# Optimization experiments

Hardware: AMD Instinct MI355X
Metric: run time of the kernel (lower is better)

Reference implementation:

```python
import jax, jax.numpy as jnp
import numpy as np

B, T, S, D, H, HD, DFF, NB = 2, 2048, 2048, 768, 12, 64, 3072, 32
HID = H * HD
EPS = 1e-6
NEG = -1e9


def rmsnorm(x, w):
    # T5 RMSNorm: no mean subtraction, no bias
    var = jnp.mean(jnp.square(x), axis=-1, keepdims=True)
    return x * jax.lax.rsqrt(var + EPS) * w


def sdpa(h, kv, m, wq, wk, wv, wo):
    # h: [B,Tq,D], kv: [B,Tk,D], m: additive mask broadcastable to [B,H,Tq,Tk]
    b, tq, _ = h.shape
    tk = kv.shape[1]
    q = (h @ wq).reshape(b, tq, H, HD)
    k = (kv @ wk).reshape(b, tk, H, HD)
    v = (kv @ wv).reshape(b, tk, H, HD)
    scores = jnp.einsum('bthd,bshd->bhts', q, k) + m  # scale=1.0 (T5)
    p = jax.nn.softmax(scores, axis=-1)
    y = jnp.einsum('bhts,bshd->bthd', p, v).reshape(b, tq, HID)
    return y @ wo


def setup_inputs() -> dict:
    key = jax.random.key(0)
    ks = jax.random.split(key, 16)
    x = jax.random.normal(ks[0], (B, T, D), dtype=jnp.float32)
    # causal additive mask for decoder self-attention
    causal = jnp.tril(jnp.ones((T, T), dtype=bool))
    mask = jnp.broadcast_to(jnp.where(causal, 0.0, NEG)[None, None], (B, 1, T, T)).astype(jnp.float32)
    relative_position = jax.random.randint(ks[1], (1, 1, T, T), 0, NB)
    encoder_hidden_states = jax.random.normal(ks[2], (B, S, D), dtype=jnp.float32)
    encoder_attention_mask = jnp.zeros((B, 1, T, S), dtype=jnp.float32)
    sc = 0.02
    p = {
        'sn_w': jnp.ones((D,), jnp.float32),
        'wq': sc * jax.random.normal(ks[3], (D, HID)),
        'wk': sc * jax.random.normal(ks[4], (D, HID)),
        'wv': sc * jax.random.normal(ks[5], (D, HID)),
        'wo': sc * jax.random.normal(ks[6], (HID, D)),
        'rel_emb': sc * jax.random.normal(ks[7], (NB, H)),
        'cn_w': jnp.ones((D,), jnp.float32),
        'cwq': sc * jax.random.normal(ks[8], (D, HID)),
        'cwk': sc * jax.random.normal(ks[9], (D, HID)),
        'cwv': sc * jax.random.normal(ks[10], (D, HID)),
        'cwo': sc * jax.random.normal(ks[11], (HID, D)),
        'pn_w': jnp.ones((D,), jnp.float32),
        'ffn_wi': sc * jax.random.normal(ks[12], (D, DFF)),
        'ffn_wo': sc * jax.random.normal(ks[13], (DFF, D)),
    }
    return dict(x=x, mask=mask, relative_position=relative_position,
                encoder_hidden_states=encoder_hidden_states,
                encoder_attention_mask=encoder_attention_mask, **p)


def reference(x, mask, relative_position, encoder_hidden_states, encoder_attention_mask,
              sn_w, wq, wk, wv, wo, rel_emb, cn_w, cwq, cwk, cwv, cwo, pn_w, ffn_wi, ffn_wo):
    # self-attention with relative-position bias added into additive mask
    h = rmsnorm(x, sn_w)
    # rel_emb[relative_position]: [1,1,T,T,H] -> permute(0,1,4,2,3) -> squeeze(0) -> [1,H,T,T]
    position_bias = jnp.transpose(rel_emb[relative_position], (0, 1, 4, 2, 3))[0]
    self_mask = mask + position_bias
    y = sdpa(h, h, self_mask, wq, wk, wv, wo)
    attn_out = y + x
    # cross-attention (no relative bias -> zeros position bias)
    enc_dec_position_bias = jnp.zeros_like(encoder_attention_mask)
    h2 = rmsnorm(attn_out, cn_w)
    y2 = sdpa(h2, encoder_hidden_states, encoder_attention_mask + enc_dec_position_bias,
              cwq, cwk, cwv, cwo)
    attn_out = y2 + attn_out
    # T5 FFN: relu(x @ wi) @ wo, pre-norm, residual
    hn = rmsnorm(attn_out, pn_w)
    ff = jax.nn.relu(hn @ ffn_wi) @ ffn_wo
    return (attn_out + ff, position_bias, enc_dec_position_bias)
```

## Files before the change

kernel.cpp:

```cpp
#include <hip/hip_runtime.h>
#include <hip/hip_bf16.h>
#include <stdint.h>

#define T5_B   2
#define T5_T   2048
#define T5_S   2048
#define T5_D   768
#define T5_H   12
#define T5_HD  64
#define T5_DFF 3072
#define T5_NB  32
#define NROW   4096

#define LOG2E 1.4426950408889634f

typedef __attribute__((ext_vector_type(8))) short bf16x8;
typedef __attribute__((ext_vector_type(4))) short short4v;
typedef __attribute__((ext_vector_type(4))) float f32x4;
typedef __attribute__((ext_vector_type(16))) float f32x16;

__device__ __forceinline__ unsigned short f2bf(float x) {
  unsigned int u = __float_as_uint(x);
  unsigned int r = (u + 0x7FFFu + ((u >> 16) & 1u)) >> 16;
  return (unsigned short)r;
}

__device__ __forceinline__ float fexp2(float x) {
  float d;
  asm("v_exp_f32 %0, %1" : "=v"(d) : "v"(x));
  return d;
}

__device__ __forceinline__ void load_lds16(const void* g, void* l) {
  __builtin_amdgcn_global_load_lds(
      (__attribute__((address_space(1))) void*)(const_cast<void*>(g)),
      (__attribute__((address_space(3))) void*)(l), 16, 0, 0);
}

__device__ __forceinline__ unsigned cvt_pk_bf16(float lo_, float hi_) {
  unsigned d;
  asm("v_cvt_pk_bf16_f32 %0, %1, %2" : "=v"(d) : "v"(lo_), "v"(hi_));
  return d;
}

__device__ __forceinline__ f32x4 mfma16(short4v a, short4v b, f32x4 c) {
#if __has_builtin(__builtin_amdgcn_mfma_f32_16x16x16bf16_1k)
  return __builtin_amdgcn_mfma_f32_16x16x16bf16_1k(a, b, c, 0, 0, 0);
#else
  asm volatile("v_mfma_f32_16x16x16_bf16 %0, %1, %2, %0" : "+v"(c) : "v"(a), "v"(b));
  return c;
#endif
}

__device__ __forceinline__ int xcd_swz(int f, int nwg) {
  int q8 = nwg >> 3, r8 = nwg & 7, xcd = f & 7, base = f >> 3;
  return (xcd < r8 ? xcd * (q8 + 1) : r8 * (q8 + 1) + (xcd - r8) * q8) + base;
}

template <int TM, int TN, int EPI, int NBUF>
__device__ __forceinline__ void gemm_body(
    int f, int gx, int nwg,
    const unsigned short* __restrict__ A, const unsigned short* __restrict__ Bt,
    void* __restrict__ C, const float* __restrict__ res, int N, int K,
    unsigned short* LDS, unsigned short* vtp = nullptr, int vcol0 = 0, int qe = 0) {
  constexpr bool USE32 = (TM >= 128 && TN >= 128);
  constexpr int WR = (TM >= 128) ? 2 : 1;
  constexpr int WC = 4 / WR;
  constexpr int AM = TM / WR / 16;
  constexpr int AN = TN / WC / 16;
  constexpr int CHA = TM / 8, CHB = TN / 8, CPW = (CHA + CHB) / 4;
  constexpr int BUFSH = (TM + TN) * 64;
  constexpr int DEPTH = NBUF - 1;
  const int tid = threadIdx.x, lane = tid & 63, wv = tid >> 6;
  const int lo = lane & 15, hi = lane >> 4;
  const int l5 = lane >> 5, l31 = lane & 31;
  const int wr = wv / WC, wc = wv % WC;
  const int wg = xcd_swz(f, nwg);
  const int m0 = (wg / gx) * TM, n0 = (wg % gx) * TN;

  f32x4 acc[USE32 ? 1 : AM][USE32 ? 1 : AN];
  f32x16 acc32[USE32 ? 2 : 1][USE32 ? 2 : 1];
  if (USE32) {
#pragma unroll
    for (int i = 0; i < (USE32 ? 2 : 1); ++i)
#pragma unroll
      for (int j = 0; j < (USE32 ? 2 : 1); ++j)
#pragma unroll
        for (int r = 0; r < 16; ++r) acc32[i][j][r] = 0.f;
  } else {
#pragma unroll
    for (int i = 0; i < (USE32 ? 1 : AM); ++i)
#pragma unroll
      for (int j = 0; j < (USE32 ? 1 : AN); ++j) acc[i][j] = f32x4{0.f, 0.f, 0.f, 0.f};
  }

  const int srr  = lane >> 3;
  const int scol = ((lane & 7) ^ srr) * 8;

  auto stage = [&](int k0, int bsel) {
    unsigned short* Ab = LDS + bsel * BUFSH;
    unsigned short* Bb = Ab + TM * 64;
#pragma unroll
    for (int j = 0; j < CPW; ++j) {
      int c = wv * CPW + j;
      if (c < CHA)
        load_lds16(A + (size_t)(m0 + c * 8 + srr) * K + k0 + scol, Ab + c * 512);
      else {
        int c2 = c - CHA;
        load_lds16(Bt + (size_t)(n0 + c2 * 8 + srr) * K + k0 + scol, Bb + c2 * 512);
      }
    }
  };

  const int nIt = K >> 6;
#pragma unroll
  for (int p = 0; p < DEPTH; ++p)
    if (p < nIt) stage(p << 6, p % NBUF);

  for (int it = 0; it < nIt; ++it) {
    const int bsel = it % NBUF;
    if (NBUF == 1) {
      stage(it << 6, 0);
      asm volatile("s_waitcnt vmcnt(0)" ::: "memory");
    } else if (it + DEPTH < nIt) {
      stage((it + DEPTH) << 6, (it + DEPTH) % NBUF);
      asm volatile("s_waitcnt vmcnt(%0)" :: "n"(DEPTH * CPW) : "memory");
    } else if (it + 1 < nIt) {
      asm volatile("s_waitcnt vmcnt(%0)" :: "n"(CPW) : "memory");
    } else {
      asm volatile("s_waitcnt vmcnt(0)" ::: "memory");
    }
    __builtin_amdgcn_s_barrier();
    __builtin_amdgcn_sched_barrier(0);
    const unsigned short* Ab = LDS + bsel * BUFSH;
    const unsigned short* Bb = Ab + TM * 64;
    if (USE32) {
#pragma unroll
      for (int kk = 0; kk < 4; ++kk) {
        bf16x8 af[2], bfr[2];
#pragma unroll
        for (int i = 0; i < 2; ++i) {
          int row = wr * 64 + i * 32 + l31;
          unsigned by = (unsigned)(row * 128) + ((unsigned)(((kk * 2 + l5) ^ (row & 7))) << 4);
          af[i] = *(const bf16x8*)((const char*)Ab + by);
        }
#pragma unroll
        for (int j = 0; j < 2; ++j) {
          int row = wc * 64 + j * 32 + l31;
          unsigned by = (unsigned)(row * 128) + ((unsigned)(((kk * 2 + l5) ^ (row & 7))) << 4);
          bfr[j] = *(const bf16x8*)((const char*)Bb + by);
        }
        __builtin_amdgcn_s_setprio(1);
#pragma unroll
        for (int i = 0; i < 2; ++i)
#pragma unroll
          for (int j = 0; j < 2; ++j)
            acc32[i][j] = __builtin_amdgcn_mfma_f32_32x32x16_bf16(af[i], bfr[j], acc32[i][j], 0, 0, 0);
        __builtin_amdgcn_s_setprio(0);
      }
    } else {
#pragma unroll
      for (int kk = 0; kk < 2; ++kk) {
        bf16x8 af[AM], bfr[AN];
#pragma unroll
        for (int i = 0; i < AM; ++i) {
          int row = wr * (AM * 16) + i * 16 + lo;
          unsigned by = (unsigned)(row * 128) + ((unsigned)(((kk * 4 + hi) ^ (row & 7))) << 4);
          af[i] = *(const bf16x8*)((const char*)Ab + by);
        }
#pragma unroll
        for (int j = 0; j < AN; ++j) {
          int row = wc * (AN * 16) + j * 16 + lo;
          unsigned by = (unsigned)(row * 128) + ((unsigned)(((kk * 4 + hi) ^ (row & 7))) << 4);
          bfr[j] = *(const bf16x8*)((const char*)Bb + by);
        }
        __builtin_amdgcn_s_setprio(1);
#pragma unroll
        for (int i = 0; i < AM; ++i)
#pragma unroll
          for (int j = 0; j < AN; ++j)
            acc[i][j] = __builtin_amdgcn_mfma_f32_16x16x32_bf16(af[i], bfr[j], acc[i][j], 0, 0, 0);
        __builtin_amdgcn_s_setprio(0);
      }
    }
    __builtin_amdgcn_sched_barrier(0);
    __builtin_amdgcn_s_barrier();
  }

  if (USE32) {
#pragma unroll
    for (int i = 0; i < 2; ++i)
#pragma unroll
      for (int j = 0; j < 2; ++j) {
        int colb = n0 + wc * 64 + j * 32 + l31;
#pragma unroll
        for (int g = 0; g < 4; ++g) {
          int rowb = m0 + wr * 64 + i * 32 + g * 8 + 4 * l5;
          if (EPI == 3 && colb >= vcol0) {
            int cc = colb - vcol0, hh = cc >> 6, dd = cc & 63;
            int bb = rowb >> 11, tt = rowb & 2047;
            unsigned long long pk = (unsigned long long)f2bf(acc32[i][j][g * 4 + 0])
                                  | ((unsigned long long)f2bf(acc32[i][j][g * 4 + 1]) << 16)
                                  | ((unsigned long long)f2bf(acc32[i][j][g * 4 + 2]) << 32)
                                  | ((unsigned long long)f2bf(acc32[i][j][g * 4 + 3]) << 48);
            *(unsigned long long*)(vtp + ((size_t)((bb * 12 + hh) * 64 + dd)) * 2048 + tt) = pk;
          } else {
#pragma unroll
            for (int rr = 0; rr < 4; ++rr) {
              float v = acc32[i][j][g * 4 + rr];
              size_t idx = (size_t)(rowb + rr) * N + colb;
              if (EPI == 3) {
                if (colb < qe) v *= LOG2E;
                ((unsigned short*)C)[idx] = f2bf(v);
              } else if (EPI == 0) {
                ((unsigned short*)C)[idx] = f2bf(v);
              } else if (EPI == 1) {
                ((float*)C)[idx] = v + res[idx];
              } else if (EPI == 2) {
                ((unsigned short*)C)[idx] = f2bf(fmaxf(v, 0.0f));
              } else {
                ((unsigned short*)C)[idx] = f2bf(v * LOG2E);
              }
            }
          }
        }
      }
  } else {
#pragma unroll
    for (int mi = 0; mi < (USE32 ? 1 : AM); ++mi)
#pragma unroll
      for (int ni = 0; ni < (USE32 ? 1 : AN); ++ni) {
        int row = m0 + wr * (AM * 16) + mi * 16 + hi * 4;
        int col = n0 + wc * (AN * 16) + ni * 16 + lo;
#pragma unroll
        for (int r = 0; r < 4; ++r) {
          float v = acc[mi][ni][r];
          size_t idx = (size_t)(row + r) * N + col;
          if (EPI == 0 || EPI == 3) {
            ((unsigned short*)C)[idx] = f2bf(v);
          } else if (EPI == 1) {
            ((float*)C)[idx] = v + res[idx];
          } else if (EPI == 2) {
            ((unsigned short*)C)[idx] = f2bf(fmaxf(v, 0.0f));
          } else {
            ((unsigned short*)C)[idx] = f2bf(v * LOG2E);
          }
        }
      }
  }
}

template <int TM, int TN, int EPI, int NBUF>
__global__ __launch_bounds__(256)
void gemm_bt(const unsigned short* __restrict__ A, const unsigned short* __restrict__ Bt,
             void* __restrict__ C, const float* __restrict__ res, int N, int K) {
  __shared__ __align__(16) unsigned short LDS[NBUF * (TM + TN) * 64];
  int f = blockIdx.y * gridDim.x + blockIdx.x;
  gemm_body<TM, TN, EPI, NBUF>(f, gridDim.x, gridDim.x * gridDim.y, A, Bt, C, res, N, K, LDS);
}

struct PrepArgs {
  const float* wsrc[10];
  unsigned short* wdst[10];
  const float* enc; unsigned short* encb;
  const int* rp; unsigned char* rp8;
  const float* x; const float* snw; unsigned short* normb;
};

__global__ __launch_bounds__(256)
void prep_kernel(PrepArgs a) {
  __shared__ __align__(16) float tile[32][33];
  const int bid = blockIdx.x, tid = threadIdx.x;
  if (bid < 9216) {
    int widx, rem, Kd, Nd;
    if (bid < 4608)      { widx = bid / 576; rem = bid % 576;  Kd = 768;  Nd = 768;  }
    else if (bid < 6912) { widx = 8;         rem = bid - 4608; Kd = 768;  Nd = 3072; }
    else                 { widx = 9;         rem = bid - 6912; Kd = 3072; Nd = 768;  }
    const float* W = a.wsrc[widx];
    unsigned short* Wt = a.wdst[widx];
    int nb = Nd / 32;
    int n0 = (rem % nb) * 32, k0 = (rem / nb) * 32;
    int tx = tid & 31, ty = tid >> 5;
#pragma unroll
    for (int i = 0; i < 32; i += 8)
      tile[ty + i][tx] = W[(size_t)(k0 + ty + i) * Nd + n0 + tx];
    __syncthreads();
#pragma unroll
    for (int i = 0; i < 32; i += 8)
      Wt[(size_t)(n0 + ty + i) * Kd + k0 + tx] = f2bf(tile[tx][ty + i]);
  } else if (bid < 12288) {
    int i = (bid - 9216) * 256 + tid;
    float4 v = ((const float4*)a.enc)[i];
    unsigned long long pk = (unsigned long long)f2bf(v.x)
                          | ((unsigned long long)f2bf(v.y) << 16)
                          | ((unsigned long long)f2bf(v.z) << 32)
                          | ((unsigned long long)f2bf(v.w) << 48);
    *(unsigned long long*)(a.encb + (size_t)i * 4) = pk;
  } else if (bid < 13312) {
    int idx = (bid - 12288) * 256 + tid;
    const int4* src = (const int4*)(a.rp + (size_t)idx * 16);
    int4 v0 = src[0], v1 = src[1], v2 = src[2], v3 = src[3];
    uint4 o;
    o.x = (v0.x & 31) | ((v0.y & 31) << 8) | ((v0.z & 31) << 16) | ((v0.w & 31) << 24);
    o.y = (v1.x & 31) | ((v1.y & 31) << 8) | ((v1.z & 31) << 16) | ((v1.w & 31) << 24);
    o.z = (v2.x & 31) | ((v2.y & 31) << 8) | ((v2.z & 31) << 16) | ((v2.w & 31) << 24);
    o.w = (v3.x & 31) | ((v3.y & 31) << 8) | ((v3.z & 31) << 16) | ((v3.w & 31) << 24);
    ((uint4*)a.rp8)[idx] = o;
  } else {
    int row = bid - 13312;
    const float* r = a.x + (size_t)row * 768;
    float x0 = r[tid], x1 = r[tid + 256], x2 = r[tid + 512];
    float s = x0 * x0 + x1 * x1 + x2 * x2;
#pragma unroll
    for (int off = 32; off > 0; off >>= 1) s += __shfl_xor(s, off);
    float* wsm = &tile[0][0];
    int lane = tid & 63, wvv = tid >> 6;
    if (lane == 0) wsm[wvv] = s;
    __syncthreads();
    float tot = wsm[0] + wsm[1] + wsm[2] + wsm[3];
    float rinv = rsqrtf(tot * (1.0f / 768.0f) + 1e-6f);
    unsigned short* o = a.normb + (size_t)row * 768;
    o[tid]       = f2bf(x0 * rinv * a.snw[tid]);
    o[tid + 256] = f2bf(x1 * rinv * a.snw[tid + 256]);
    o[tid + 512] = f2bf(x2 * rinv * a.snw[tid + 512]);
  }
}

__global__ __launch_bounds__(256)
void rmsnorm_kernel(const float* __restrict__ in, const float* __restrict__ w,
                    unsigned short* __restrict__ out) {
  int row = blockIdx.x, tid = threadIdx.x;
  const float* r = in + (size_t)row * 768;
  float x0 = r[tid], x1 = r[tid + 256], x2 = r[tid + 512];
  float s = x0 * x0 + x1 * x1 + x2 * x2;
#pragma unroll
  for (int off = 32; off > 0; off >>= 1) s += __shfl_xor(s, off);
  __shared__ float ws_[4];
  int lane = tid & 63, wv = tid >> 6;
  if (lane == 0) ws_[wv] = s;
  __syncthreads();
  float tot = ws_[0] + ws_[1] + ws_[2] + ws_[3];
  float rinv = rsqrtf(tot * (1.0f / 768.0f) + 1e-6f);
  unsigned short* o = out + (size_t)row * 768;
  o[tid]       = f2bf(x0 * rinv * w[tid]);
  o[tid + 256] = f2bf(x1 * rinv * w[tid + 256]);
  o[tid + 512] = f2bf(x2 * rinv * w[tid + 512]);
}

struct Stage1Args {
  const unsigned short *normb, *wqkvT, *encb, *wckvT;
  unsigned short *qkv, *ckv, *vT1, *vT2;
  const int* rp; const float* rel;
  float *out1, *out2;
};

__global__ __launch_bounds__(256)
void stage1_kernel(Stage1Args a) {
  __shared__ __align__(16) unsigned short LDS[16384];
  const int bid = blockIdx.x, tid = threadIdx.x;
  if (bid < 576) {
    gemm_body<128, 128, 3, 1>(bid, 18, 576, a.normb, a.wqkvT, a.qkv, nullptr, 2304, 768,
                              LDS, a.vT1, 1536, 768);
  } else if (bid < 960) {
    gemm_body<128, 128, 3, 1>(bid - 576, 12, 384, a.encb, a.wckvT, a.ckv, nullptr, 1536, 768,
                              LDS, a.vT2, 768, 0);
  } else {
    const int p = bid - 960;
    float* rl = (float*)LDS;
    for (int i = tid; i < 384; i += 256) rl[i] = a.rel[i];
    __syncthreads();
    int t = p >> 1;
    int s = (p & 1) * 1024 + tid * 4;
    int4 nb = *(const int4*)(a.rp + (size_t)t * 2048 + s);
#pragma unroll
    for (int h = 0; h < 12; ++h) {
      float4 v = make_float4(rl[nb.x * 12 + h], rl[nb.y * 12 + h],
                             rl[nb.z * 12 + h], rl[nb.w * 12 + h]);
      *(float4*)(a.out1 + ((size_t)h * 2048 + t) * 2048 + s) = v;
    }
    size_t zbase = ((size_t)p * 256 + tid) * 8;
    float4 z = make_float4(0.f, 0.f, 0.f, 0.f);
    *(float4*)(a.out2 + zbase)     = z;
    *(float4*)(a.out2 + zbase + 4) = z;
  }
}

template <bool SELF>
__device__ __forceinline__ void attn_qcomp(
    const bf16x8& qf0, const bf16x8& qf1, f32x4* Oc, float& l_,
    const unsigned* nb4, const float* rel_l, int qrow, bool edge, int s0,
    const unsigned short* Kb, const unsigned short* Vb, int lo, int hi) {
  f32x4 S[4];
  __builtin_amdgcn_s_setprio(1);
#pragma unroll
  for (int ct = 0; ct < 4; ++ct) {
    int krow = ct * 16 + lo;
    unsigned by0 = ((unsigned)(krow * 128 + hi * 16))      ^ ((unsigned)(krow & 7) << 4);
    unsigned by1 = ((unsigned)(krow * 128 + 64 + hi * 16)) ^ ((unsigned)(krow & 7) << 4);
    bf16x8 kf0 = *(const bf16x8*)((const char*)Kb + by0);
    bf16x8 kf1 = *(const bf16x8*)((const char*)Kb + by1);
    f32x4 sa = f32x4{0.f, 0.f, 0.f, 0.f};
    sa = __builtin_amdgcn_mfma_f32_16x16x32_bf16(kf0, qf0, sa, 0, 0, 0);
    sa = __builtin_amdgcn_mfma_f32_16x16x32_bf16(kf1, qf1, sa, 0, 0, 0);
    S[ct] = sa;
  }
  __builtin_amdgcn_s_setprio(0);

  if constexpr (SELF) {
#pragma unroll
    for (int ct = 0; ct < 4; ++ct) {
#pragma unroll
      for (int r = 0; r < 4; ++r) {
        int s = s0 + ct * 16 + hi * 4 + r;
        float sc = S[ct][r] + rel_l[(nb4[ct] >> (8 * r)) & 31u];
        if (edge && s > qrow) sc = -1e30f;
        S[ct][r] = sc;
      }
    }
  }

  float rs = 0.f;
#pragma unroll
  for (int ct = 0; ct < 4; ++ct)
#pragma unroll
    for (int r = 0; r < 4; ++r) { float e = fexp2(S[ct][r]); S[ct][r] = e; rs += e; }
  l_ += rs;

  short4v pf[4];
#pragma unroll
  for (int ct = 0; ct < 4; ++ct) {
    union { unsigned u[2]; short4v s; } cv;
    cv.u[0] = cvt_pk_bf16(S[ct][0], S[ct][1]);
    cv.u[1] = cvt_pk_bf16(S[ct][2], S[ct][3]);
    pf[ct] = cv.s;
  }

  __builtin_amdgcn_s_setprio(1);
#pragma unroll
  for (int dt = 0; dt < 4; ++dt) {
    int vrow = dt * 16 + lo;
#pragma unroll
    for (int ct = 0; ct < 4; ++ct) {
      unsigned vb = ((unsigned)(vrow * 128 + ct * 32 + hi * 8)) ^ ((unsigned)(vrow & 7) << 4);
      short4v vf = *(const short4v*)((const char*)Vb + vb);
      Oc[dt] = mfma16(vf, pf[ct], Oc[dt]);
    }
  }
  __builtin_amdgcn_s_setprio(0);
}

__device__ __forceinline__ void attn_store(f32x4* Oc, float l_, unsigned short* yr) {
  l_ += __shfl_xor(l_, 16);
  l_ += __shfl_xor(l_, 32);
  float inv = 1.0f / l_;
#pragma unroll
  for (int dt = 0; dt < 4; ++dt) {
    unsigned long long pk = (unsigned long long)f2bf(Oc[dt][0] * inv)
                          | ((unsigned long long)f2bf(Oc[dt][1] * inv) << 16)
                          | ((unsigned long long)f2bf(Oc[dt][2] * inv) << 32)
                          | ((unsigned long long)f2bf(Oc[dt][3] * inv) << 48);
    *(unsigned long long*)(yr + dt * 16) = pk;
  }
}

__global__ __launch_bounds__(256)
void attn_self_kernel(const unsigned short* __restrict__ qp,
                      const unsigned short* __restrict__ kp,
                      const unsigned short* __restrict__ vT,
                      const unsigned char* __restrict__ rp8,
                      const float* __restrict__ rel_emb,
                      unsigned short* __restrict__ yp) {
  __shared__ __align__(16) unsigned short Kls[2][4096];
  __shared__ __align__(16) unsigned short Vls[2][4096];
  __shared__ float rel_l[32];

  const int tid = threadIdx.x, lane = tid & 63, wv = tid >> 6;
  const int lo = lane & 15, hi = lane >> 4;
  const int wg = xcd_swz(blockIdx.x + 16 * (blockIdx.y + 12 * blockIdx.z), 384);
  const int xq = wg & 15, h = (wg >> 4) % 12, b = (wg >> 4) / 12;
  const int qta = xq, qtb = 31 - xq;
  const int ntiles = qtb + 1;

  if (tid < 32) rel_l[tid] = rel_emb[tid * 12 + h] * LOG2E;

  const int qA = qta * 64 + wv * 16 + lo;
  const int qB = qtb * 64 + wv * 16 + lo;
  const unsigned short* qrA = qp + (size_t)(b * T5_T + qA) * 2304 + h * 64 + hi * 8;
  const unsigned short* qrB = qp + (size_t)(b * T5_T + qB) * 2304 + h * 64 + hi * 8;
  const bf16x8 qa0 = *(const bf16x8*)qrA;
  const bf16x8 qa1 = *(const bf16x8*)(qrA + 32);
  const bf16x8 qb0 = *(const bf16x8*)qrB;
  const bf16x8 qb1 = *(const bf16x8*)(qrB + 32);
  const unsigned char* rpqA = rp8 + (size_t)qA * 2048 + hi * 4;
  const unsigned char* rpqB = rp8 + (size_t)qB * 2048 + hi * 4;

  f32x4 OA[4], OB[4];
  float lA = 0.f, lB = 0.f;
#pragma unroll
  for (int i = 0; i < 4; ++i) { OA[i] = f32x4{0.f, 0.f, 0.f, 0.f}; OB[i] = f32x4{0.f, 0.f, 0.f, 0.f}; }

  const int krr = lane >> 3;
  const int kd0 = ((lane & 7) ^ krr) * 8;

  auto stage = [&](int kt, int bsel) {
    const int s0 = kt * 64;
#pragma unroll
    for (int j = 0; j < 2; ++j) {
      int c = wv * 2 + j;
      int rr = c * 8 + krr;
      load_lds16(kp + (size_t)(b * 2048 + s0 + rr) * 2304 + h * 64 + kd0, &Kls[bsel][c * 512]);
      load_lds16(vT + (size_t)((b * 12 + h) * 64 + rr) * 2048 + s0 + kd0,  &Vls[bsel][c * 512]);
    }
  };

  stage(0, 0);

  for (int kt = 0; kt < ntiles; ++kt) {
    const int bsel = kt & 1;
    const int s0 = kt * 64;
    asm volatile("s_waitcnt vmcnt(0)" ::: "memory");
    __syncthreads();
    unsigned nbA[4], nbB[4];
    if (kt <= qta) {
#pragma unroll
      for (int ct = 0; ct < 4; ++ct) nbA[ct] = *(const unsigned*)(rpqA + s0 + ct * 16);
    }
#pragma unroll
    for (int ct = 0; ct < 4; ++ct) nbB[ct] = *(const unsigned*)(rpqB + s0 + ct * 16);
    if (kt + 1 < ntiles) stage(kt + 1, bsel ^ 1);

    const unsigned short* Kb = &Kls[bsel][0];
    const unsigned short* Vb = &Vls[bsel][0];

    if (kt <= qta)
      attn_qcomp<true>(qa0, qa1, OA, lA, nbA, rel_l, qA, kt == qta, s0, Kb, Vb, lo, hi);
    attn_qcomp<true>(qb0, qb1, OB, lB, nbB, rel_l, qB, kt == qtb, s0, Kb, Vb, lo, hi);
  }

#if !__has_builtin(__builtin_amdgcn_mfma_f32_16x16x16bf16_1k)
  asm volatile("s_nop 7\n\ts_nop 7" ::: );
#endif

  attn_store(OA, lA, yp + (size_t)(b * T5_T + qA) * 768 + h * 64 + hi * 4);
  attn_store(OB, lB, yp + (size_t)(b * T5_T + qB) * 768 + h * 64 + hi * 4);
}

__global__ __launch_bounds__(256)
void attn_cross_kernel(const unsigned short* __restrict__ qp,
                       const unsigned short* __restrict__ kp,
                       const unsigned short* __restrict__ vT,
                       unsigned short* __restrict__ yp) {
  __shared__ __align__(16) unsigned short Kls[2][4096];
  __shared__ __align__(16) unsigned short Vls[2][4096];

  const int tid = threadIdx.x, lane = tid & 63, wv = tid >> 6;
  const int lo = lane & 15, hi = lane >> 4;
  const int wg = xcd_swz(blockIdx.x + 16 * (blockIdx.y + 12 * blockIdx.z), 384);
  const int xq = wg & 15, h = (wg >> 4) % 12, b = (wg >> 4) / 12;

  const int qA = (xq * 2) * 64 + wv * 16 + lo;
  const int qB = (xq * 2 + 1) * 64 + wv * 16 + lo;
  const unsigned short* qrA = qp + (size_t)(b * T5_T + qA) * 768 + h * 64 + hi * 8;
  const unsigned short* qrB = qp + (size_t)(b * T5_T + qB) * 768 + h * 64 + hi * 8;
  const bf16x8 qa0 = *(const bf16x8*)qrA;
  const bf16x8 qa1 = *(const bf16x8*)(qrA + 32);
  const bf16x8 qb0 = *(const bf16x8*)qrB;
  const bf16x8 qb1 = *(const bf16x8*)(qrB + 32);

  f32x4 OA[4], OB[4];
  float lA = 0.f, lB = 0.f;
#pragma unroll
  for (int i = 0; i < 4; ++i) { OA[i] = f32x4{0.f, 0.f, 0.f, 0.f}; OB[i] = f32x4{0.f, 0.f, 0.f, 0.f}; }

  const int krr = lane >> 3;
  const int kd0 = ((lane & 7) ^ krr) * 8;

  auto stage = [&](int kt, int bsel) {
    const int s0 = kt * 64;
#pragma unroll
    for (int j = 0; j < 2; ++j) {
      int c = wv * 2 + j;
      int rr = c * 8 + krr;
      load_lds16(kp + (size_t)(b * 2048 + s0 + rr) * 1536 + h * 64 + kd0, &Kls[bsel][c * 512]);
      load_lds16(vT + (size_t)((b * 12 + h) * 64 + rr) * 2048 + s0 + kd0, &Vls[bsel][c * 512]);
    }
  };

  stage(0, 0);

  for (int kt = 0; kt < 32; ++kt) {
    const int bsel = kt & 1;
    asm volatile("s_waitcnt vmcnt(0)" ::: "memory");
    __syncthreads();
    if (kt + 1 < 32) stage(kt + 1, bsel ^ 1);
    const unsigned short* Kb = &Kls[bsel][0];
    const unsigned short* Vb = &Vls[bsel][0];
    attn_qcomp<false>(qa0, qa1, OA, lA, nullptr, nullptr, 0, false, kt * 64, Kb, Vb, lo, hi);
    attn_qcomp<false>(qb0, qb1, OB, lB, nullptr, nullptr, 0, false, kt * 64, Kb, Vb, lo, hi);
  }

#if !__has_builtin(__builtin_amdgcn_mfma_f32_16x16x16bf16_1k)
  asm volatile("s_nop 7\n\ts_nop 7" ::: );
#endif

  attn_store(OA, lA, yp + (size_t)(b * T5_T + qA) * 768 + h * 64 + hi * 4);
  attn_store(OB, lB, yp + (size_t)(b * T5_T + qB) * 768 + h * 64 + hi * 4);
}

extern "C" void kernel_launch(void* const* d_in, const int* in_sizes, int n_in,
                              void* d_out, int out_size, void* d_ws, size_t ws_size,
                              hipStream_t stream) {
  (void)in_sizes; (void)n_in; (void)out_size; (void)ws_size;
  const float* x    = (const float*)d_in[0];
  const int*   rp   = (const int*)d_in[2];
  const float* enc  = (const float*)d_in[3];
  const float* sn_w = (const float*)d_in[5];
  const float* wq   = (const float*)d_in[6];
  const float* wk   = (const float*)d_in[7];
  const float* wvw  = (const float*)d_in[8];
  const float* wo   = (const float*)d_in[9];
  const float* rel  = (const float*)d_in[10];
  const float* cn_w = (const float*)d_in[11];
  const float* cwq  = (const float*)d_in[12];
  const float* cwk  = (const float*)d_in[13];
  const float* cwv  = (const float*)d_in[14];
  const float* cwo  = (const float*)d_in[15];
  const float* pn_w = (const float*)d_in[16];
  const float* wi   = (const float*)d_in[17];
  const float* wo2  = (const float*)d_in[18];

  float* out0 = (float*)d_out;
  float* out1 = out0 + (size_t)NROW * T5_D;
  float* out2 = out1 + (size_t)T5_H * T5_T * T5_T;

  char* ws = (char*)d_ws;
  size_t off = 0;
  auto alloc = [&](size_t bytes) { char* p = ws + off; off += (bytes + 255) & ~(size_t)255; return p; };
  unsigned short* wqkvT = (unsigned short*)alloc((size_t)2304 * 768 * 2);
  unsigned short* woT   = (unsigned short*)alloc((size_t)768 * 768 * 2);
  unsigned short* wckvT = (unsigned short*)alloc((size_t)1536 * 768 * 2);
  unsigned short* wcqT  = (unsigned short*)alloc((size_t)768 * 768 * 2);
  unsigned short* wcoT  = (unsigned short*)alloc((size_t)768 * 768 * 2);
  unsigned short* wiT   = (unsigned short*)alloc((size_t)3072 * 768 * 2);
  unsigned short* woT2  = (unsigned short*)alloc((size_t)768 * 3072 * 2);
  unsigned short* normb = (unsigned short*)alloc((size_t)NROW * 768 * 2);
  unsigned short* encb  = (unsigned short*)alloc((size_t)NROW * 768 * 2);
  unsigned short* ybuf  = (unsigned short*)alloc((size_t)NROW * 768 * 2);
  unsigned short* cq    = (unsigned short*)alloc((size_t)NROW * 768 * 2);
  float*          attn  = (float*)alloc((size_t)NROW * 768 * 4);
  unsigned char*  rp8p  = (unsigned char*)alloc((size_t)2048 * 2048);
  unsigned short* qkv   = (unsigned short*)alloc((size_t)NROW * 2304 * 2);
  unsigned short* ckv   = (unsigned short*)alloc((size_t)NROW * 1536 * 2);
  unsigned short* vT1   = (unsigned short*)alloc((size_t)24 * 64 * 2048 * 2);
  unsigned short* vT2   = (unsigned short*)alloc((size_t)24 * 64 * 2048 * 2);
  unsigned short* ffh   = (unsigned short*)alloc((size_t)NROW * 3072 * 2);

  dim3 blk(256);

  {
    PrepArgs pa;
    pa.wsrc[0] = wq;  pa.wdst[0] = wqkvT;
    pa.wsrc[1] = wk;  pa.wdst[1] = wqkvT + 768 * 768;
    pa.wsrc[2] = wvw; pa.wdst[2] = wqkvT + 2 * 768 * 768;
    pa.wsrc[3] = wo;  pa.wdst[3] = woT;
    pa.wsrc[4] = cwk; pa.wdst[4] = wckvT;
    pa.wsrc[5] = cwv; pa.wdst[5] = wckvT + 768 * 768;
    pa.wsrc[6] = cwq; pa.wdst[6] = wcqT;
    pa.wsrc[7] = cwo; pa.wdst[7] = wcoT;
    pa.wsrc[8] = wi;  pa.wdst[8] = wiT;
    pa.wsrc[9] = wo2; pa.wdst[9] = woT2;
    pa.enc = enc; pa.encb = encb; pa.rp = rp; pa.rp8 = rp8p;
    pa.x = x; pa.snw = sn_w; pa.normb = normb;
    prep_kernel<<<17408, blk, 0, stream>>>(pa);
  }

  {
    Stage1Args sa;
    sa.normb = normb; sa.wqkvT = wqkvT; sa.encb = encb; sa.wckvT = wckvT;
    sa.qkv = qkv; sa.ckv = ckv; sa.vT1 = vT1; sa.vT2 = vT2;
    sa.rp = rp; sa.rel = rel; sa.out1 = out1; sa.out2 = out2;
    stage1_kernel<<<5056, blk, 0, stream>>>(sa);
  }

  attn_self_kernel<<<dim3(16, 12, 2), blk, 0, stream>>>(qkv, qkv + 768, vT1, rp8p, rel, ybuf);
  gemm_bt<64, 64, 1, 3><<<dim3(12, 64), blk, 0, stream>>>(ybuf, woT, attn, x, 768, 768);

  rmsnorm_kernel<<<NROW, blk, 0, stream>>>(attn, cn_w, normb);
  gemm_bt<64, 64, 4, 3><<<dim3(12, 64), blk, 0, stream>>>(normb, wcqT, cq, nullptr, 768, 768);
  attn_cross_kernel<<<dim3(16, 12, 2), blk, 0, stream>>>(cq, ckv, vT2, ybuf);
  gemm_bt<64, 64, 1, 3><<<dim3(12, 64), blk, 0, stream>>>(ybuf, wcoT, attn, attn, 768, 768);

  rmsnorm_kernel<<<NROW, blk, 0, stream>>>(attn, pn_w, normb);
  gemm_bt<128, 128, 2, 1><<<dim3(24, 32), blk, 0, stream>>>(normb, wiT, ffh, nullptr, 3072, 768);
  gemm_bt<64, 64, 1, 3><<<dim3(12, 64), blk, 0, stream>>>(ffh, woT2, out0, attn, 768, 3072);
}
```

Before: 340.9 us.

## Split attention query tiles across 512-thread blocks and defer weight prep to stage1

The self- and cross-attention kernels move from 256-thread blocks, where each wave handled two query tiles in sequence, to 512-thread blocks, where each group of four waves owns one query tile. This gives more waves per block to hide latency and halves the per-wave serial work and register footprint, while each K/V tile staged in LDS is still shared by both query tiles. Transposing the weights that are not needed for the first GEMMs (wo, cwq, cwo, ffn) and packing the relative positions are moved out of the prep kernel into the stage1 kernel, so they overlap with the QKV GEMMs instead of delaying them. In the causal kernel the waves on the short query tile sit idle for the later key tiles, and the larger blocks may reduce occupancy.

```diff
diff --git a/kernel.cpp b/kernel.cpp
--- a/kernel.cpp
+++ b/kernel.cpp
@@ -55,6 +55,22 @@
 __device__ __forceinline__ int xcd_swz(int f, int nwg) {
   int q8 = nwg >> 3, r8 = nwg & 7, xcd = f & 7, base = f >> 3;
   return (xcd < r8 ? xcd * (q8 + 1) : r8 * (q8 + 1) + (xcd - r8) * q8) + base;
+}
+
+__device__ __forceinline__ void wtrans_tile(const float* __restrict__ W,
+                                            unsigned short* __restrict__ Wt,
+                                            int rem, int Kd, int Nd,
+                                            float (*tile)[33], int tid) {
+  int nb = Nd / 32;
+  int n0 = (rem % nb) * 32, k0 = (rem / nb) * 32;
+  int tx = tid & 31, ty = tid >> 5;
+#pragma unroll
+  for (int i = 0; i < 32; i += 8)
+    tile[ty + i][tx] = W[(size_t)(k0 + ty + i) * Nd + n0 + tx];
+  __syncthreads();
+#pragma unroll
+  for (int i = 0; i < 32; i += 8)
+    Wt[(size_t)(n0 + ty + i) * Kd + k0 + tx] = f2bf(tile[tx][ty + i]);
 }
 
 template <int TM, int TN, int EPI, int NBUF>
@@ -260,10 +276,9 @@
 }
 
 struct PrepArgs {
-  const float* wsrc[10];
-  unsigned short* wdst[10];
+  const float* wsrc[5];
+  unsigned short* wdst[5];
   const float* enc; unsigned short* encb;
-  const int* rp; unsigned char* rp8;
   const float* x; const float* snw; unsigned short* normb;
 };
 
@@ -271,43 +286,19 @@
 void prep_kernel(PrepArgs a) {
   __shared__ __align__(16) float tile[32][33];
   const int bid = blockIdx.x, tid = threadIdx.x;
-  if (bid < 9216) {
-    int widx, rem, Kd, Nd;
-    if (bid < 4608)      { widx = bid / 576; rem = bid % 576;  Kd = 768;  Nd = 768;  }
-    else if (bid < 6912) { widx = 8;         rem = bid - 4608; Kd = 768;  Nd = 3072; }
-    else                 { widx = 9;         rem = bid - 6912; Kd = 3072; Nd = 768;  }
-    const float* W = a.wsrc[widx];
-    unsigned short* Wt = a.wdst[widx];
-    int nb = Nd / 32;
-    int n0 = (rem % nb) * 32, k0 = (rem / nb) * 32;
-    int tx = tid & 31, ty = tid >> 5;
-#pragma unroll
-    for (int i = 0; i < 32; i += 8)
-      tile[ty + i][tx] = W[(size_t)(k0 + ty + i) * Nd + n0 + tx];
-    __syncthreads();
-#pragma unroll
-    for (int i = 0; i < 32; i += 8)
-      Wt[(size_t)(n0 + ty + i) * Kd + k0 + tx] = f2bf(tile[tx][ty + i]);
-  } else if (bid < 12288) {
-    int i = (bid - 9216) * 256 + tid;
+  if (bid < 2880) {
+    int widx = bid / 576, rem = bid % 576;
+    wtrans_tile(a.wsrc[widx], a.wdst[widx], rem, 768, 768, tile, tid);
+  } else if (bid < 5952) {
+    int i = (bid - 2880) * 256 + tid;
     float4 v = ((const float4*)a.enc)[i];
     unsigned long long pk = (unsigned long long)f2bf(v.x)
                           | ((unsigned long long)f2bf(v.y) << 16)
                           | ((unsigned long long)f2bf(v.z) << 32)
                           | ((unsigned long long)f2bf(v.w) << 48);
     *(unsigned long long*)(a.encb + (size_t)i * 4) = pk;
-  } else if (bid < 13312) {
-    int idx = (bid - 12288) * 256 + tid;
-    const int4* src = (const int4*)(a.rp + (size_t)idx * 16);
-    int4 v0 = src[0], v1 = src[1], v2 = src[2], v3 = src[3];
-    uint4 o;
-    o.x = (v0.x & 31) | ((v0.y & 31) << 8) | ((v0.z & 31) << 16) | ((v0.w & 31) << 24);
-    o.y = (v1.x & 31) | ((v1.y & 31) << 8) | ((v1.z & 31) << 16) | ((v1.w & 31) << 24);
-    o.z = (v2.x & 31) | ((v2.y & 31) << 8) | ((v2.z & 31) << 16) | ((v2.w & 31) << 24);
-    o.w = (v3.x & 31) | ((v3.y & 31) << 8) | ((v3.z & 31) << 16) | ((v3.w & 31) << 24);
-    ((uint4*)a.rp8)[idx] = o;
   } else {
-    int row = bid - 13312;
+    int row = bid - 5952;
     const float* r = a.x + (size_t)row * 768;
     float x0 = r[tid], x1 = r[tid + 256], x2 = r[tid + 512];
     float s = x0 * x0 + x1 * x1 + x2 * x2;
@@ -352,6 +343,9 @@
   unsigned short *qkv, *ckv, *vT1, *vT2;
   const int* rp; const float* rel;
   float *out1, *out2;
+  const float *wo, *cwq, *cwo, *wi, *wo2;
+  unsigned short *woT, *wcqT, *wcoT, *wiT, *woT2;
+  unsigned char* rp8;
 };
 
 __global__ __launch_bounds__(256)
@@ -364,7 +358,7 @@
   } else if (bid < 960) {
     gemm_body<128, 128, 3, 1>(bid - 576, 12, 384, a.encb, a.wckvT, a.ckv, nullptr, 1536, 768,
                               LDS, a.vT2, 768, 0);
-  } else {
+  } else if (bid < 5056) {
     const int p = bid - 960;
     float* rl = (float*)LDS;
     for (int i = tid; i < 384; i += 256) rl[i] = a.rel[i];
@@ -382,6 +376,26 @@
     float4 z = make_float4(0.f, 0.f, 0.f, 0.f);
     *(float4*)(a.out2 + zbase)     = z;
     *(float4*)(a.out2 + zbase + 4) = z;
+  } else if (bid < 5632) {
+    wtrans_tile(a.wo,  a.woT,  bid - 5056, 768, 768, (float(*)[33])LDS, tid);
+  } else if (bid < 6208) {
+    wtrans_tile(a.cwq, a.wcqT, bid - 5632, 768, 768, (float(*)[33])LDS, tid);
+  } else if (bid < 6784) {
+    wtrans_tile(a.cwo, a.wcoT, bid - 6208, 768, 768, (float(*)[33])LDS, tid);
+  } else if (bid < 9088) {
+    wtrans_tile(a.wi,  a.wiT,  bid - 6784, 768, 3072, (float(*)[33])LDS, tid);
+  } else if (bid < 11392) {
+    wtrans_tile(a.wo2, a.woT2, bid - 9088, 3072, 768, (float(*)[33])LDS, tid);
+  } else {
+    int idx = (bid - 11392) * 256 + tid;
+    const int4* src = (const int4*)(a.rp + (size_t)idx * 16);
+    int4 v0 = src[0], v1 = src[1], v2 = src[2], v3 = src[3];
+    uint4 o;
+    o.x = (v0.x & 31) | ((v0.y & 31) << 8) | ((v0.z & 31) << 16) | ((v0.w & 31) << 24);
+    o.y = (v1.x & 31) | ((v1.y & 31) << 8) | ((v1.z & 31) << 16) | ((v1.w & 31) << 24);
+    o.z = (v2.x & 31) | ((v2.y & 31) << 8) | ((v2.z & 31) << 16) | ((v2.w & 31) << 24);
+    o.w = (v3.x & 31) | ((v3.y & 31) << 8) | ((v3.z & 31) << 16) | ((v3.w & 31) << 24);
+    ((uint4*)a.rp8)[idx] = o;
   }
 }
 
@@ -463,7 +477,7 @@
   }
 }
 
-__global__ __launch_bounds__(256)
+__global__ __launch_bounds__(512)
 void attn_self_kernel(const unsigned short* __restrict__ qp,
                       const unsigned short* __restrict__ kp,
                       const unsigned short* __restrict__ vT,
@@ -476,41 +490,34 @@
 
   const int tid = threadIdx.x, lane = tid & 63, wv = tid >> 6;
   const int lo = lane & 15, hi = lane >> 4;
+  const int qset = wv >> 2, wq = wv & 3;
   const int wg = xcd_swz(blockIdx.x + 16 * (blockIdx.y + 12 * blockIdx.z), 384);
   const int xq = wg & 15, h = (wg >> 4) % 12, b = (wg >> 4) / 12;
   const int qta = xq, qtb = 31 - xq;
   const int ntiles = qtb + 1;
+  const int qt = qset ? qtb : qta;
 
   if (tid < 32) rel_l[tid] = rel_emb[tid * 12 + h] * LOG2E;
 
-  const int qA = qta * 64 + wv * 16 + lo;
-  const int qB = qtb * 64 + wv * 16 + lo;
-  const unsigned short* qrA = qp + (size_t)(b * T5_T + qA) * 2304 + h * 64 + hi * 8;
-  const unsigned short* qrB = qp + (size_t)(b * T5_T + qB) * 2304 + h * 64 + hi * 8;
-  const bf16x8 qa0 = *(const bf16x8*)qrA;
-  const bf16x8 qa1 = *(const bf16x8*)(qrA + 32);
-  const bf16x8 qb0 = *(const bf16x8*)qrB;
-  const bf16x8 qb1 = *(const bf16x8*)(qrB + 32);
-  const unsigned char* rpqA = rp8 + (size_t)qA * 2048 + hi * 4;
-  const unsigned char* rpqB = rp8 + (size_t)qB * 2048 + hi * 4;
-
-  f32x4 OA[4], OB[4];
-  float lA = 0.f, lB = 0.f;
-#pragma unroll
-  for (int i = 0; i < 4; ++i) { OA[i] = f32x4{0.f, 0.f, 0.f, 0.f}; OB[i] = f32x4{0.f, 0.f, 0.f, 0.f}; }
+  const int q = qt * 64 + wq * 16 + lo;
+  const unsigned short* qr = qp + (size_t)(b * T5_T + q) * 2304 + h * 64 + hi * 8;
+  const bf16x8 qf0 = *(const bf16x8*)qr;
+  const bf16x8 qf1 = *(const bf16x8*)(qr + 32);
+  const unsigned char* rpq = rp8 + (size_t)q * 2048 + hi * 4;
+
+  f32x4 Oc[4];
+  float l_ = 0.f;
+#pragma unroll
+  for (int i = 0; i < 4; ++i) Oc[i] = f32x4{0.f, 0.f, 0.f, 0.f};
 
   const int krr = lane >> 3;
   const int kd0 = ((lane & 7) ^ krr) * 8;
 
   auto stage = [&](int kt, int bsel) {
     const int s0 = kt * 64;
-#pragma unroll
-    for (int j = 0; j < 2; ++j) {
-      int c = wv * 2 + j;
-      int rr = c * 8 + krr;
-      load_lds16(kp + (size_t)(b * 2048 + s0 + rr) * 2304 + h * 64 + kd0, &Kls[bsel][c * 512]);
-      load_lds16(vT + (size_t)((b * 12 + h) * 64 + rr) * 2048 + s0 + kd0,  &Vls[bsel][c * 512]);
-    }
+    int rr = wv * 8 + krr;
+    load_lds16(kp + (size_t)(b * 2048 + s0 + rr) * 2304 + h * 64 + kd0, &Kls[bsel][wv * 512]);
+    load_lds16(vT + (size_t)((b * 12 + h) * 64 + rr) * 2048 + s0 + kd0,  &Vls[bsel][wv * 512]);
   };
 
   stage(0, 0);
@@ -520,32 +527,27 @@
     const int s0 = kt * 64;
     asm volatile("s_waitcnt vmcnt(0)" ::: "memory");
     __syncthreads();
-    unsigned nbA[4], nbB[4];
-    if (kt <= qta) {
-#pragma unroll
-      for (int ct = 0; ct < 4; ++ct) nbA[ct] = *(const unsigned*)(rpqA + s0 + ct * 16);
+    const bool active = qset || (kt <= qta);
+    unsigned nb4[4];
+    if (active) {
+#pragma unroll
+      for (int ct = 0; ct < 4; ++ct) nb4[ct] = *(const unsigned*)(rpq + s0 + ct * 16);
     }
-#pragma unroll
-    for (int ct = 0; ct < 4; ++ct) nbB[ct] = *(const unsigned*)(rpqB + s0 + ct * 16);
     if (kt + 1 < ntiles) stage(kt + 1, bsel ^ 1);
 
-    const unsigned short* Kb = &Kls[bsel][0];
-    const unsigned short* Vb = &Vls[bsel][0];
-
-    if (kt <= qta)
-      attn_qcomp<true>(qa0, qa1, OA, lA, nbA, rel_l, qA, kt == qta, s0, Kb, Vb, lo, hi);
-    attn_qcomp<true>(qb0, qb1, OB, lB, nbB, rel_l, qB, kt == qtb, s0, Kb, Vb, lo, hi);
+    if (active)
+      attn_qcomp<true>(qf0, qf1, Oc, l_, nb4, rel_l, q, kt == qt, s0,
+                       &Kls[bsel][0], &Vls[bsel][0], lo, hi);
   }
 
 #if !__has_builtin(__builtin_amdgcn_mfma_f32_16x16x16bf16_1k)
   asm volatile("s_nop 7\n\ts_nop 7" ::: );
 #endif
 
-  attn_store(OA, lA, yp + (size_t)(b * T5_T + qA) * 768 + h * 64 + hi * 4);
-  attn_store(OB, lB, yp + (size_t)(b * T5_T + qB) * 768 + h * 64 + hi * 4);
-}
-
-__global__ __launch_bounds__(256)
+  attn_store(Oc, l_, yp + (size_t)(b * T5_T + q) * 768 + h * 64 + hi * 4);
+}
+
+__global__ __launch_bounds__(512)
 void attn_cross_kernel(const unsigned short* __restrict__ qp,
                        const unsigned short* __restrict__ kp,
                        const unsigned short* __restrict__ vT,
@@ -555,35 +557,28 @@
 
   const int tid = threadIdx.x, lane = tid & 63, wv = tid >> 6;
   const int lo = lane & 15, hi = lane >> 4;
+  const int qset = wv >> 2, wq = wv & 3;
   const int wg = xcd_swz(blockIdx.x + 16 * (blockIdx.y + 12 * blockIdx.z), 384);
   const int xq = wg & 15, h = (wg >> 4) % 12, b = (wg >> 4) / 12;
 
-  const int qA = (xq * 2) * 64 + wv * 16 + lo;
-  const int qB = (xq * 2 + 1) * 64 + wv * 16 + lo;
-  const unsigned short* qrA = qp + (size_t)(b * T5_T + qA) * 768 + h * 64 + hi * 8;
-  const unsigned short* qrB = qp + (size_t)(b * T5_T + qB) * 768 + h * 64 + hi * 8;
-  const bf16x8 qa0 = *(const bf16x8*)qrA;
-  const bf16x8 qa1 = *(const bf16x8*)(qrA + 32);
-  const bf16x8 qb0 = *(const bf16x8*)qrB;
-  const bf16x8 qb1 = *(const bf16x8*)(qrB + 32);
-
-  f32x4 OA[4], OB[4];
-  float lA = 0.f, lB = 0.f;
-#pragma unroll
-  for (int i = 0; i < 4; ++i) { OA[i] = f32x4{0.f, 0.f, 0.f, 0.f}; OB[i] = f32x4{0.f, 0.f, 0.f, 0.f}; }
+  const int q = (xq * 2 + qset) * 64 + wq * 16 + lo;
+  const unsigned short* qr = qp + (size_t)(b * T5_T + q) * 768 + h * 64 + hi * 8;
+  const bf16x8 qf0 = *(const bf16x8*)qr;
+  const bf16x8 qf1 = *(const bf16x8*)(qr + 32);
+
+  f32x4 Oc[4];
+  float l_ = 0.f;
+#pragma unroll
+  for (int i = 0; i < 4; ++i) Oc[i] = f32x4{0.f, 0.f, 0.f, 0.f};
 
   const int krr = lane >> 3;
   const int kd0 = ((lane & 7) ^ krr) * 8;
 
   auto stage = [&](int kt, int bsel) {
     const int s0 = kt * 64;
-#pragma unroll
-    for (int j = 0; j < 2; ++j) {
-      int c = wv * 2 + j;
-      int rr = c * 8 + krr;
-      load_lds16(kp + (size_t)(b * 2048 + s0 + rr) * 1536 + h * 64 + kd0, &Kls[bsel][c * 512]);
-      load_lds16(vT + (size_t)((b * 12 + h) * 64 + rr) * 2048 + s0 + kd0, &Vls[bsel][c * 512]);
-    }
+    int rr = wv * 8 + krr;
+    load_lds16(kp + (size_t)(b * 2048 + s0 + rr) * 1536 + h * 64 + kd0, &Kls[bsel][wv * 512]);
+    load_lds16(vT + (size_t)((b * 12 + h) * 64 + rr) * 2048 + s0 + kd0, &Vls[bsel][wv * 512]);
   };
 
   stage(0, 0);
@@ -593,18 +588,15 @@
     asm volatile("s_waitcnt vmcnt(0)" ::: "memory");
     __syncthreads();
     if (kt + 1 < 32) stage(kt + 1, bsel ^ 1);
-    const unsigned short* Kb = &Kls[bsel][0];
-    const unsigned short* Vb = &Vls[bsel][0];
-    attn_qcomp<false>(qa0, qa1, OA, lA, nullptr, nullptr, 0, false, kt * 64, Kb, Vb, lo, hi);
-    attn_qcomp<false>(qb0, qb1, OB, lB, nullptr, nullptr, 0, false, kt * 64, Kb, Vb, lo, hi);
+    attn_qcomp<false>(qf0, qf1, Oc, l_, nullptr, nullptr, 0, false, kt * 64,
+                      &Kls[bsel][0], &Vls[bsel][0], lo, hi);
   }
 
 #if !__has_builtin(__builtin_amdgcn_mfma_f32_16x16x16bf16_1k)
   asm volatile("s_nop 7\n\ts_nop 7" ::: );
 #endif
 
-  attn_store(OA, lA, yp + (size_t)(b * T5_T + qA) * 768 + h * 64 + hi * 4);
-  attn_store(OB, lB, yp + (size_t)(b * T5_T + qB) * 768 + h * 64 + hi * 4);
+  attn_store(Oc, l_, yp + (size_t)(b * T5_T + q) * 768 + h * 64 + hi * 4);
 }
 
 extern "C" void kernel_launch(void* const* d_in, const int* in_sizes, int n_in,
@@ -662,16 +654,11 @@
     pa.wsrc[0] = wq;  pa.wdst[0] = wqkvT;
     pa.wsrc[1] = wk;  pa.wdst[1] = wqkvT + 768 * 768;
     pa.wsrc[2] = wvw; pa.wdst[2] = wqkvT + 2 * 768 * 768;
-    pa.wsrc[3] = wo;  pa.wdst[3] = woT;
-    pa.wsrc[4] = cwk; pa.wdst[4] = wckvT;
-    pa.wsrc[5] = cwv; pa.wdst[5] = wckvT + 768 * 768;
-    pa.wsrc[6] = cwq; pa.wdst[6] = wcqT;
-    pa.wsrc[7] = cwo; pa.wdst[7] = wcoT;
-    pa.wsrc[8] = wi;  pa.wdst[8] = wiT;
-    pa.wsrc[9] = wo2; pa.wdst[9] = woT2;
-    pa.enc = enc; pa.encb = encb; pa.rp = rp; pa.rp8 = rp8p;
+    pa.wsrc[3] = cwk; pa.wdst[3] = wckvT;
+    pa.wsrc[4] = cwv; pa.wdst[4] = wckvT + 768 * 768;
+    pa.enc = enc; pa.encb = encb;
     pa.x = x; pa.snw = sn_w; pa.normb = normb;
-    prep_kernel<<<17408, blk, 0, stream>>>(pa);
+    prep_kernel<<<10048, blk, 0, stream>>>(pa);
   }
 
   {
@@ -679,15 +666,18 @@
     sa.normb = normb; sa.wqkvT = wqkvT; sa.encb = encb; sa.wckvT = wckvT;
     sa.qkv = qkv; sa.ckv = ckv; sa.vT1 = vT1; sa.vT2 = vT2;
     sa.rp = rp; sa.rel = rel; sa.out1 = out1; sa.out2 = out2;
-    stage1_kernel<<<5056, blk, 0, stream>>>(sa);
-  }
-
-  attn_self_kernel<<<dim3(16, 12, 2), blk, 0, stream>>>(qkv, qkv + 768, vT1, rp8p, rel, ybuf);
+    sa.wo = wo; sa.cwq = cwq; sa.cwo = cwo; sa.wi = wi; sa.wo2 = wo2;
+    sa.woT = woT; sa.wcqT = wcqT; sa.wcoT = wcoT; sa.wiT = wiT; sa.woT2 = woT2;
+    sa.rp8 = rp8p;
+    stage1_kernel<<<12416, blk, 0, stream>>>(sa);
+  }
+
+  attn_self_kernel<<<dim3(16, 12, 2), dim3(512), 0, stream>>>(qkv, qkv + 768, vT1, rp8p, rel, ybuf);
   gemm_bt<64, 64, 1, 3><<<dim3(12, 64), blk, 0, stream>>>(ybuf, woT, attn, x, 768, 768);
 
   rmsnorm_kernel<<<NROW, blk, 0, stream>>>(attn, cn_w, normb);
   gemm_bt<64, 64, 4, 3><<<dim3(12, 64), blk, 0, stream>>>(normb, wcqT, cq, nullptr, 768, 768);
-  attn_cross_kernel<<<dim3(16, 12, 2), blk, 0, stream>>>(cq, ckv, vT2, ybuf);
+  attn_cross_kernel<<<dim3(16, 12, 2), dim3(512), 0, stream>>>(cq, ckv, vT2, ybuf);
   gemm_bt<64, 64, 1, 3><<<dim3(12, 64), blk, 0, stream>>>(ybuf, wcoT, attn, attn, 768, 768);
 
   rmsnorm_kernel<<<NROW, blk, 0, stream>>>(attn, pn_w, normb);
```

Result: faster. 322.5 us (median of 3 runs) (-5.4%).
